# Optimization experiments

Measured on AMD Instinct MI355X. Metric: run time of the kernel, lower is better.

## Reference

```python
import jax, jax.numpy as jnp
import numpy as np

B, S, E = 8, 1024, 512
H = 8            # num_heads
D = E // H       # head_dim
FFN = 2048
WINDOW = 5       # local_window_size
EPS = 1e-5


def _mha(x, in_w, in_b, out_w, out_b, mask=None):
    """PyTorch nn.MultiheadAttention (batch_first) forward. mask: True = blocked."""
    b, s, e = x.shape
    qkv = x @ in_w.T + in_b                      # [B,S,3E]
    q, k, v = jnp.split(qkv, 3, axis=-1)
    def heads(t):
        return t.reshape(b, s, H, D).transpose(0, 2, 1, 3)  # [B,H,S,D]
    q, k, v = heads(q), heads(k), heads(v)
    scores = jnp.einsum('bhsd,bhtd->bhst', q, k) / np.sqrt(D).astype(x.dtype)
    if mask is not None:
        scores = jnp.where(mask[None, None], -jnp.inf, scores)
    attn = jax.nn.softmax(scores, axis=-1)
    out = jnp.einsum('bhst,bhtd->bhsd', attn, v)  # [B,H,S,D]
    out = out.transpose(0, 2, 1, 3).reshape(b, s, e)
    return out @ out_w.T + out_b


def _layernorm(x, g, b):
    mu = jnp.mean(x, axis=-1, keepdims=True)
    var = jnp.mean(jnp.square(x - mu), axis=-1, keepdims=True)
    return (x - mu) * jax.lax.rsqrt(var + EPS) * g + b


def setup_inputs() -> dict:
    key = jax.random.key(0)
    ks = jax.random.split(key, 8)
    w = 0.02  # weight scale for numerical sanity
    return {
        'x': jax.random.normal(ks[0], (B, S, E), jnp.float32),
        'l_in_w': jax.random.normal(ks[1], (3 * E, E), jnp.float32) * w,
        'l_in_b': jnp.zeros((3 * E,), jnp.float32),
        'l_out_w': jax.random.normal(ks[2], (E, E), jnp.float32) * w,
        'l_out_b': jnp.zeros((E,), jnp.float32),
        'g_in_w': jax.random.normal(ks[3], (3 * E, E), jnp.float32) * w,
        'g_in_b': jnp.zeros((3 * E,), jnp.float32),
        'g_out_w': jax.random.normal(ks[4], (E, E), jnp.float32) * w,
        'g_out_b': jnp.zeros((E,), jnp.float32),
        'ffn_w1': jax.random.normal(ks[5], (FFN, E), jnp.float32) * w,
        'ffn_b1': jnp.zeros((FFN,), jnp.float32),
        'ffn_w2': jax.random.normal(ks[6], (E, FFN), jnp.float32) * w,
        'ffn_b2': jnp.zeros((E,), jnp.float32),
        'ln1_g': jnp.ones((E,), jnp.float32),
        'ln1_b': jnp.zeros((E,), jnp.float32),
        'ln2_g': jnp.ones((E,), jnp.float32),
        'ln2_b': jnp.zeros((E,), jnp.float32),
    }


def reference(x, l_in_w, l_in_b, l_out_w, l_out_b,
              g_in_w, g_in_b, g_out_w, g_out_b,
              ffn_w1, ffn_b1, ffn_w2, ffn_b2,
              ln1_g, ln1_b, ln2_g, ln2_b):
    s = x.shape[1]
    idx = jnp.arange(s)
    local_mask = jnp.abs(idx[:, None] - idx[None, :]) > WINDOW  # True = blocked
    local_out = _mha(x, l_in_w, l_in_b, l_out_w, l_out_b, mask=local_mask)
    global_out = _mha(x, g_in_w, g_in_b, g_out_w, g_out_b)
    x = x + local_out + global_out
    x = _layernorm(x, ln1_g, ln1_b)
    ffn = jax.nn.relu(x @ ffn_w1.T + ffn_b1) @ ffn_w2.T + ffn_b2
    x = _layernorm(x + ffn, ln2_g, ln2_b)
    return x
```

## Files before the change

### kernel.cpp

```cpp
#include <hip/hip_runtime.h>
#include <hip/hip_bf16.h>
#include <stdint.h>

#define Bb 8
#define Ss 1024
#define Ee 512
#define Hh 8
#define Dh 64
#define FFNd 2048
#define EPSv 1e-5f

typedef float f32x4 __attribute__((ext_vector_type(4)));
typedef int   i32x4 __attribute__((ext_vector_type(4)));

__device__ inline float bf2f(ushort u) {
    uint32_t x = ((uint32_t)u) << 16; float f; __builtin_memcpy(&f, &x, 4); return f;
}
__device__ inline ushort f2bf(float f) {
    uint32_t x; __builtin_memcpy(&x, &f, 4);
    uint32_t r = (x + 0x7FFFu + ((x >> 16) & 1u)) >> 16; return (ushort)r;
}

__device__ inline void gload16(const ushort* g, ushort* l) {
    __builtin_amdgcn_global_load_lds((const __attribute__((address_space(1))) void*)g,
                                     (__attribute__((address_space(3))) void*)l,
                                     16, 0, 0);
}

__global__ void cvt_f32_bf16(const float* __restrict__ in, ushort* __restrict__ out, int n4) {
    int i = blockIdx.x * blockDim.x + threadIdx.x;
    if (i < n4) {
        float4 v = ((const float4*)in)[i];
        ushort4 o;
        o.x = f2bf(v.x); o.y = f2bf(v.y); o.z = f2bf(v.z); o.w = f2bf(v.w);
        ((ushort4*)out)[i] = o;
    }
}

template<bool OUT_BF16, bool RELU>
__global__ __launch_bounds__(256) void gemm_bt(const ushort* __restrict__ A,
                                               const ushort* __restrict__ Bm,
                                               const float* __restrict__ bias,
                                               void* __restrict__ C,
                                               int M, int N, int K) {
    __shared__ ushort Alds[128 * 32];
    __shared__ ushort Blds[128 * 32];
    int tid  = threadIdx.x;
    int lane = tid & 63, w = tid >> 6;
    int wr = w >> 1, wc = w & 1;
    int g  = lane >> 4, fr = lane & 15;
    int m0 = blockIdx.y * 128, n0 = blockIdx.x * 128;

    int lr4 = lane >> 2;
    int lc8 = (lane & 3) * 8;
    const ushort* gA0 = A  + (size_t)(m0 + (w * 2) * 16 + lr4) * K + lc8;
    const ushort* gA1 = gA0 + (size_t)16 * K;
    const ushort* gB0 = Bm + (size_t)(n0 + (w * 2) * 16 + lr4) * K + lc8;
    const ushort* gB1 = gB0 + (size_t)16 * K;
    ushort* lA0 = Alds + (w * 2) * 16 * 32;
    ushort* lA1 = lA0 + 16 * 32;
    ushort* lB0 = Blds + (w * 2) * 16 * 32;
    ushort* lB1 = lB0 + 16 * 32;

    f32x4 acc[4][4] = {};

    for (int kb = 0; kb < K; kb += 32) {
        __syncthreads();
        gload16(gA0 + kb, lA0);
        gload16(gA1 + kb, lA1);
        gload16(gB0 + kb, lB0);
        gload16(gB1 + kb, lB1);
        __syncthreads();
        i32x4 af[4], bfr[4];
        #pragma unroll
        for (int mt = 0; mt < 4; ++mt)
            af[mt] = *(const i32x4*)(Alds + (wr * 64 + mt * 16 + fr) * 32 + g * 8);
        #pragma unroll
        for (int nt = 0; nt < 4; ++nt)
            bfr[nt] = *(const i32x4*)(Blds + (wc * 64 + nt * 16 + fr) * 32 + g * 8);
        #pragma unroll
        for (int mt = 0; mt < 4; ++mt)
            #pragma unroll
            for (int nt = 0; nt < 4; ++nt)
                asm("v_mfma_f32_16x16x32_bf16 %0, %1, %2, %0"
                    : "+v"(acc[mt][nt]) : "v"(af[mt]), "v"(bfr[nt]));
    }

    #pragma unroll
    for (int mt = 0; mt < 4; ++mt) {
        int r0 = m0 + wr * 64 + mt * 16 + g * 4;
        #pragma unroll
        for (int nt = 0; nt < 4; ++nt) {
            int c = n0 + wc * 64 + nt * 16 + fr;
            float bv = bias[c];
            #pragma unroll
            for (int r = 0; r < 4; ++r) {
                float v = acc[mt][nt][r] + bv;
                if (RELU) v = v > 0.f ? v : 0.f;
                if (OUT_BF16) ((ushort*)C)[(size_t)(r0 + r) * N + c] = f2bf(v);
                else          ((float*)C)[(size_t)(r0 + r) * N + c] = v;
            }
        }
    }
}

__global__ __launch_bounds__(256) void attn_local_mfma(const ushort* __restrict__ qkv,
                                                       ushort* __restrict__ out) {
    __shared__ ushort Klds[64 * 64];
    __shared__ ushort Vtlds[64 * 64];
    __shared__ ushort Plds[4][32 * 64];
    int tid  = threadIdx.x;
    int lane = tid & 63, w = tid >> 6;
    int fr = lane & 15, g = lane >> 4;
    int qtile = blockIdx.x & 7;
    int bh = blockIdx.x >> 3;
    int h = bh & 7, b = bh >> 3;
    const size_t bbase = (size_t)b * Ss * (3 * Ee);
    const ushort* qp = qkv + bbase + h * Dh;
    const ushort* kbase = qkv + bbase + Ee + h * Dh;
    const ushort* vbase = qkv + bbase + 2 * Ee + h * Dh;

    i32x4 qf[2][2];
    int q0 = qtile * 128 + w * 32;
    #pragma unroll
    for (int mt = 0; mt < 2; ++mt)
        #pragma unroll
        for (int kb = 0; kb < 2; ++kb)
            qf[mt][kb] = *(const i32x4*)(qp + (size_t)(q0 + mt * 16 + fr) * (3 * Ee) + kb * 32 + g * 8);

    f32x4 oacc[2][4] = {};
    f32x4 lsum[2] = {};
    ushort* Pw = Plds[w];

    int tq2 = qtile * 2;
    int kt0 = tq2 > 0 ? tq2 - 1 : 0;
    int kt1 = tq2 + 2 < 16 ? tq2 + 2 : 15;
    for (int kt = kt0; kt <= kt1; ++kt) {
        int kv0 = kt * 64;
        i32x4 kr[2], vr[2];
        #pragma unroll
        for (int u = 0; u < 2; ++u) {
            int c = tid + u * 256;
            int row = c >> 3, col8 = c & 7;
            kr[u] = *(const i32x4*)(kbase + (size_t)(kv0 + row) * (3 * Ee) + col8 * 8);
            vr[u] = *(const i32x4*)(vbase + (size_t)(kv0 + row) * (3 * Ee) + col8 * 8);
        }
        __syncthreads();
        #pragma unroll
        for (int u = 0; u < 2; ++u) {
            int c = tid + u * 256;
            int row = c >> 3, col8 = c & 7;
            int kidx = (row * 64 + col8 * 8) ^ ((row & 7) << 3);
            *(i32x4*)(Klds + kidx) = kr[u];
            ushort tmp[8];
            *(i32x4*)tmp = vr[u];
            #pragma unroll
            for (int j = 0; j < 8; ++j) {
                int d = col8 * 8 + j;
                Vtlds[(d * 64 + row) ^ ((d & 7) << 3)] = tmp[j];
            }
        }
        __syncthreads();

        bool active = (kv0 <= q0 + 36) && (kv0 + 63 >= q0 - 5);
        if (active) {
            f32x4 sacc[2][4] = {};
            i32x4 kf[4][2];
            #pragma unroll
            for (int nt = 0; nt < 4; ++nt) {
                int kvl = nt * 16 + fr;
                #pragma unroll
                for (int kb = 0; kb < 2; ++kb)
                    kf[nt][kb] = *(const i32x4*)(Klds + ((kvl * 64 + kb * 32 + g * 8) ^ ((kvl & 7) << 3)));
            }
            #pragma unroll
            for (int mt = 0; mt < 2; ++mt)
                #pragma unroll
                for (int nt = 0; nt < 4; ++nt)
                    #pragma unroll
                    for (int kb = 0; kb < 2; ++kb)
                        asm("v_mfma_f32_16x16x32_bf16 %0, %1, %2, %0"
                            : "+v"(sacc[mt][nt]) : "v"(qf[mt][kb]), "v"(kf[nt][kb]));

            #pragma unroll
            for (int mt = 0; mt < 2; ++mt) {
                #pragma unroll
                for (int r = 0; r < 4; ++r) {
                    int ql = mt * 16 + g * 4 + r;
                    int sw = (ql & 7) << 3;
                    int d0 = (q0 + ql) - (kv0 + fr);
                    int d1 = d0 - 16, d2 = d0 - 32, d3 = d0 - 48;
                    float e0 = (d0 >= -5 && d0 <= 5) ? __expf(sacc[mt][0][r] * 0.125f) : 0.f;
                    float e1 = (d1 >= -5 && d1 <= 5) ? __expf(sacc[mt][1][r] * 0.125f) : 0.f;
                    float e2 = (d2 >= -5 && d2 <= 5) ? __expf(sacc[mt][2][r] * 0.125f) : 0.f;
                    float e3 = (d3 >= -5 && d3 <= 5) ? __expf(sacc[mt][3][r] * 0.125f) : 0.f;
                    Pw[(ql * 64 +  0 + fr) ^ sw] = f2bf(e0);
                    Pw[(ql * 64 + 16 + fr) ^ sw] = f2bf(e1);
                    Pw[(ql * 64 + 32 + fr) ^ sw] = f2bf(e2);
                    Pw[(ql * 64 + 48 + fr) ^ sw] = f2bf(e3);
                    lsum[mt][r] += (e0 + e1) + (e2 + e3);
                }
            }

            i32x4 pa[2][2], vf[4][2];
            #pragma unroll
            for (int mt = 0; mt < 2; ++mt) {
                int ql = mt * 16 + fr;
                #pragma unroll
                for (int kb = 0; kb < 2; ++kb)
                    pa[mt][kb] = *(const i32x4*)(Pw + ((ql * 64 + kb * 32 + g * 8) ^ ((ql & 7) << 3)));
            }
            #pragma unroll
            for (int dn = 0; dn < 4; ++dn) {
                int d = dn * 16 + fr;
                #pragma unroll
                for (int kb = 0; kb < 2; ++kb)
                    vf[dn][kb] = *(const i32x4*)(Vtlds + ((d * 64 + kb * 32 + g * 8) ^ ((d & 7) << 3)));
            }
            #pragma unroll
            for (int mt = 0; mt < 2; ++mt)
                #pragma unroll
                for (int dn = 0; dn < 4; ++dn)
                    #pragma unroll
                    for (int kb = 0; kb < 2; ++kb)
                        asm("v_mfma_f32_16x16x32_bf16 %0, %1, %2, %0"
                            : "+v"(oacc[mt][dn]) : "v"(pa[mt][kb]), "v"(vf[dn][kb]));
        }
    }

    #pragma unroll
    for (int mt = 0; mt < 2; ++mt)
        #pragma unroll
        for (int r = 0; r < 4; ++r) {
            float s = lsum[mt][r];
            s += __shfl_xor(s, 1); s += __shfl_xor(s, 2);
            s += __shfl_xor(s, 4); s += __shfl_xor(s, 8);
            lsum[mt][r] = 1.f / s;
        }

    #pragma unroll
    for (int mt = 0; mt < 2; ++mt)
        #pragma unroll
        for (int r = 0; r < 4; ++r) {
            int qg = q0 + mt * 16 + g * 4 + r;
            size_t ob = (size_t)(b * Ss + qg) * Ee + h * Dh;
            #pragma unroll
            for (int dn = 0; dn < 4; ++dn)
                out[ob + dn * 16 + fr] = f2bf(oacc[mt][dn][r] * lsum[mt][r]);
        }
}

__global__ __launch_bounds__(256) void attn_global_mfma(const ushort* __restrict__ qkv,
                                                        ushort* __restrict__ out) {
    __shared__ ushort Klds[64 * 64];
    __shared__ ushort Vtlds[64 * 64];
    __shared__ ushort Plds[4][32 * 64];
    int tid  = threadIdx.x;
    int lane = tid & 63, w = tid >> 6;
    int fr = lane & 15, g = lane >> 4;
    int qtile = blockIdx.x & 7;
    int bh = blockIdx.x >> 3;
    int h = bh & 7, b = bh >> 3;
    const size_t bbase = (size_t)b * Ss * (3 * Ee);
    const ushort* qp = qkv + bbase + h * Dh;
    const ushort* kbase = qkv + bbase + Ee + h * Dh;
    const ushort* vbase = qkv + bbase + 2 * Ee + h * Dh;

    i32x4 qf[2][2];
    int q0 = qtile * 128 + w * 32;
    #pragma unroll
    for (int mt = 0; mt < 2; ++mt)
        #pragma unroll
        for (int kb = 0; kb < 2; ++kb)
            qf[mt][kb] = *(const i32x4*)(qp + (size_t)(q0 + mt * 16 + fr) * (3 * Ee) + kb * 32 + g * 8);

    f32x4 oacc[2][4] = {};
    f32x4 lsum[2] = {};
    ushort* Pw = Plds[w];

    for (int kt = 0; kt < 16; ++kt) {
        int kv0 = kt * 64;
        i32x4 kr[2], vr[2];
        #pragma unroll
        for (int u = 0; u < 2; ++u) {
            int c = tid + u * 256;
            int row = c >> 3, col8 = c & 7;
            kr[u] = *(const i32x4*)(kbase + (size_t)(kv0 + row) * (3 * Ee) + col8 * 8);
            vr[u] = *(const i32x4*)(vbase + (size_t)(kv0 + row) * (3 * Ee) + col8 * 8);
        }
        __syncthreads();
        #pragma unroll
        for (int u = 0; u < 2; ++u) {
            int c = tid + u * 256;
            int row = c >> 3, col8 = c & 7;
            int kidx = (row * 64 + col8 * 8) ^ ((row & 7) << 3);
            *(i32x4*)(Klds + kidx) = kr[u];
            ushort tmp[8];
            *(i32x4*)tmp = vr[u];
            #pragma unroll
            for (int j = 0; j < 8; ++j) {
                int d = col8 * 8 + j;
                Vtlds[(d * 64 + row) ^ ((d & 7) << 3)] = tmp[j];
            }
        }
        __syncthreads();

        f32x4 sacc[2][4] = {};
        i32x4 kf[4][2];
        #pragma unroll
        for (int nt = 0; nt < 4; ++nt) {
            int kvl = nt * 16 + fr;
            #pragma unroll
            for (int kb = 0; kb < 2; ++kb)
                kf[nt][kb] = *(const i32x4*)(Klds + ((kvl * 64 + kb * 32 + g * 8) ^ ((kvl & 7) << 3)));
        }
        #pragma unroll
        for (int mt = 0; mt < 2; ++mt)
            #pragma unroll
            for (int nt = 0; nt < 4; ++nt)
                #pragma unroll
                for (int kb = 0; kb < 2; ++kb)
                    asm("v_mfma_f32_16x16x32_bf16 %0, %1, %2, %0"
                        : "+v"(sacc[mt][nt]) : "v"(qf[mt][kb]), "v"(kf[nt][kb]));

        #pragma unroll
        for (int mt = 0; mt < 2; ++mt) {
            #pragma unroll
            for (int r = 0; r < 4; ++r) {
                int ql = mt * 16 + g * 4 + r;
                int sw = (ql & 7) << 3;
                float e0 = __expf(sacc[mt][0][r] * 0.125f);
                float e1 = __expf(sacc[mt][1][r] * 0.125f);
                float e2 = __expf(sacc[mt][2][r] * 0.125f);
                float e3 = __expf(sacc[mt][3][r] * 0.125f);
                Pw[(ql * 64 +  0 + fr) ^ sw] = f2bf(e0);
                Pw[(ql * 64 + 16 + fr) ^ sw] = f2bf(e1);
                Pw[(ql * 64 + 32 + fr) ^ sw] = f2bf(e2);
                Pw[(ql * 64 + 48 + fr) ^ sw] = f2bf(e3);
                lsum[mt][r] += (e0 + e1) + (e2 + e3);
            }
        }

        i32x4 pa[2][2], vf[4][2];
        #pragma unroll
        for (int mt = 0; mt < 2; ++mt) {
            int ql = mt * 16 + fr;
            #pragma unroll
            for (int kb = 0; kb < 2; ++kb)
                pa[mt][kb] = *(const i32x4*)(Pw + ((ql * 64 + kb * 32 + g * 8) ^ ((ql & 7) << 3)));
        }
        #pragma unroll
        for (int dn = 0; dn < 4; ++dn) {
            int d = dn * 16 + fr;
            #pragma unroll
            for (int kb = 0; kb < 2; ++kb)
                vf[dn][kb] = *(const i32x4*)(Vtlds + ((d * 64 + kb * 32 + g * 8) ^ ((d & 7) << 3)));
        }
        #pragma unroll
        for (int mt = 0; mt < 2; ++mt)
            #pragma unroll
            for (int dn = 0; dn < 4; ++dn)
                #pragma unroll
                for (int kb = 0; kb < 2; ++kb)
                    asm("v_mfma_f32_16x16x32_bf16 %0, %1, %2, %0"
                        : "+v"(oacc[mt][dn]) : "v"(pa[mt][kb]), "v"(vf[dn][kb]));
    }

    #pragma unroll
    for (int mt = 0; mt < 2; ++mt)
        #pragma unroll
        for (int r = 0; r < 4; ++r) {
            float s = lsum[mt][r];
            s += __shfl_xor(s, 1); s += __shfl_xor(s, 2);
            s += __shfl_xor(s, 4); s += __shfl_xor(s, 8);
            lsum[mt][r] = 1.f / s;
        }

    #pragma unroll
    for (int mt = 0; mt < 2; ++mt)
        #pragma unroll
        for (int r = 0; r < 4; ++r) {
            int qg = q0 + mt * 16 + g * 4 + r;
            size_t ob = (size_t)(b * Ss + qg) * Ee + h * Dh;
            #pragma unroll
            for (int dn = 0; dn < 4; ++dn)
                out[ob + dn * 16 + fr] = f2bf(oacc[mt][dn][r] * lsum[mt][r]);
        }
}

__global__ __launch_bounds__(256) void ln_add3(const float* __restrict__ x,
                                               const float* __restrict__ p1,
                                               const float* __restrict__ p2,
                                               const float* __restrict__ gam,
                                               const float* __restrict__ bet,
                                               ushort* __restrict__ yb,
                                               float* __restrict__ yf) {
    int row  = blockIdx.x * 4 + (threadIdx.x >> 6);
    int lane = threadIdx.x & 63;
    size_t off = (size_t)row * Ee + lane * 8;
    float hv[8];
    float4 a0 = *(const float4*)(x + off),  a1 = *(const float4*)(x + off + 4);
    float4 b0 = *(const float4*)(p1 + off), b1 = *(const float4*)(p1 + off + 4);
    float4 c0 = *(const float4*)(p2 + off), c1 = *(const float4*)(p2 + off + 4);
    hv[0] = a0.x + b0.x + c0.x; hv[1] = a0.y + b0.y + c0.y;
    hv[2] = a0.z + b0.z + c0.z; hv[3] = a0.w + b0.w + c0.w;
    hv[4] = a1.x + b1.x + c1.x; hv[5] = a1.y + b1.y + c1.y;
    hv[6] = a1.z + b1.z + c1.z; hv[7] = a1.w + b1.w + c1.w;
    float s = 0.f;
    #pragma unroll
    for (int i = 0; i < 8; ++i) s += hv[i];
    #pragma unroll
    for (int o = 32; o; o >>= 1) s += __shfl_xor(s, o);
    float mu = s * (1.f / Ee);
    float vs = 0.f;
    #pragma unroll
    for (int i = 0; i < 8; ++i) { float d = hv[i] - mu; vs += d * d; }
    #pragma unroll
    for (int o = 32; o; o >>= 1) vs += __shfl_xor(vs, o);
    float rs = rsqrtf(vs * (1.f / Ee) + EPSv);
    #pragma unroll
    for (int i = 0; i < 8; ++i) {
        float yv = (hv[i] - mu) * rs * gam[lane * 8 + i] + bet[lane * 8 + i];
        yf[off + i] = yv;
        yb[off + i] = f2bf(yv);
    }
}

__global__ __launch_bounds__(256) void ln_add2(const float* __restrict__ a,
                                               const float* __restrict__ bsrc,
                                               const float* __restrict__ gam,
                                               const float* __restrict__ bet,
                                               float* __restrict__ outp) {
    int row  = blockIdx.x * 4 + (threadIdx.x >> 6);
    int lane = threadIdx.x & 63;
    size_t off = (size_t)row * Ee + lane * 8;
    float hv[8];
    float4 a0 = *(const float4*)(a + off),    a1 = *(const float4*)(a + off + 4);
    float4 b0 = *(const float4*)(bsrc + off), b1 = *(const float4*)(bsrc + off + 4);
    hv[0] = a0.x + b0.x; hv[1] = a0.y + b0.y; hv[2] = a0.z + b0.z; hv[3] = a0.w + b0.w;
    hv[4] = a1.x + b1.x; hv[5] = a1.y + b1.y; hv[6] = a1.z + b1.z; hv[7] = a1.w + b1.w;
    float s = 0.f;
    #pragma unroll
    for (int i = 0; i < 8; ++i) s += hv[i];
    #pragma unroll
    for (int o = 32; o; o >>= 1) s += __shfl_xor(s, o);
    float mu = s * (1.f / Ee);
    float vs = 0.f;
    #pragma unroll
    for (int i = 0; i < 8; ++i) { float d = hv[i] - mu; vs += d * d; }
    #pragma unroll
    for (int o = 32; o; o >>= 1) vs += __shfl_xor(vs, o);
    float rs = rsqrtf(vs * (1.f / Ee) + EPSv);
    #pragma unroll
    for (int i = 0; i < 8; ++i)
        outp[off + i] = (hv[i] - mu) * rs * gam[lane * 8 + i] + bet[lane * 8 + i];
}

extern "C" void kernel_launch(void* const* d_in, const int* in_sizes, int n_in,
                              void* d_out, int out_size, void* d_ws, size_t ws_size,
                              hipStream_t stream) {
    const float* x      = (const float*)d_in[0];
    const float* l_in_w = (const float*)d_in[1];
    const float* l_in_b = (const float*)d_in[2];
    const float* l_out_w= (const float*)d_in[3];
    const float* l_out_b= (const float*)d_in[4];
    const float* g_in_w = (const float*)d_in[5];
    const float* g_in_b = (const float*)d_in[6];
    const float* g_out_w= (const float*)d_in[7];
    const float* g_out_b= (const float*)d_in[8];
    const float* ffn_w1 = (const float*)d_in[9];
    const float* ffn_b1 = (const float*)d_in[10];
    const float* ffn_w2 = (const float*)d_in[11];
    const float* ffn_b2 = (const float*)d_in[12];
    const float* ln1_g  = (const float*)d_in[13];
    const float* ln1_b  = (const float*)d_in[14];
    const float* ln2_g  = (const float*)d_in[15];
    const float* ln2_b  = (const float*)d_in[16];

    char* ws = (char*)d_ws;
    ushort* xb       = (ushort*)(ws + 0);
    ushort* wb       = (ushort*)(ws + 8388608);
    ushort* l_in_wb  = wb;
    ushort* g_in_wb  = wb + 786432;
    ushort* l_out_wb = wb + 1572864;
    ushort* g_out_wb = wb + 1835008;
    ushort* w1b      = wb + 2097152;
    ushort* w2b      = wb + 3145728;
    ushort* qkvLb    = (ushort*)(ws + 16777216);
    ushort* qkvGb    = (ushort*)(ws + 41943040);
    ushort* attnLb   = (ushort*)(ws + 67108864);
    ushort* attnGb   = (ushort*)(ws + 75497472);
    float*  projL    = (float*)(ws + 16777216);
    float*  projG    = (float*)(ws + 33554432);
    ushort* y1b      = (ushort*)(ws + 50331648);
    float*  y1f      = (float*)(ws + 58720256);
    ushort* ffn1b    = (ushort*)(ws + 16777216);
    float*  ffn2f    = (float*)(ws + 75497472);

    const int M = Bb * Ss;

    auto cvt = [&](const float* in, ushort* out, int n) {
        int n4 = n / 4;
        cvt_f32_bf16<<<dim3((n4 + 255) / 256), dim3(256), 0, stream>>>(in, out, n4);
    };
    cvt(x,       xb,       Bb * Ss * Ee);
    cvt(l_in_w,  l_in_wb,  3 * Ee * Ee);
    cvt(g_in_w,  g_in_wb,  3 * Ee * Ee);
    cvt(l_out_w, l_out_wb, Ee * Ee);
    cvt(g_out_w, g_out_wb, Ee * Ee);
    cvt(ffn_w1,  w1b,      FFNd * Ee);
    cvt(ffn_w2,  w2b,      Ee * FFNd);

    gemm_bt<true, false><<<dim3((3 * Ee) / 128, M / 128), 256, 0, stream>>>(
        xb, l_in_wb, l_in_b, qkvLb, M, 3 * Ee, Ee);
    gemm_bt<true, false><<<dim3((3 * Ee) / 128, M / 128), 256, 0, stream>>>(
        xb, g_in_wb, g_in_b, qkvGb, M, 3 * Ee, Ee);

    attn_local_mfma<<<dim3(Bb * Hh * (Ss / 128)), 256, 0, stream>>>(qkvLb, attnLb);
    attn_global_mfma<<<dim3(Bb * Hh * (Ss / 128)), 256, 0, stream>>>(qkvGb, attnGb);

    gemm_bt<false, false><<<dim3(Ee / 128, M / 128), 256, 0, stream>>>(
        attnLb, l_out_wb, l_out_b, projL, M, Ee, Ee);
    gemm_bt<false, false><<<dim3(Ee / 128, M / 128), 256, 0, stream>>>(
        attnGb, g_out_wb, g_out_b, projG, M, Ee, Ee);

    ln_add3<<<dim3(M / 4), 256, 0, stream>>>(x, projL, projG, ln1_g, ln1_b, y1b, y1f);

    gemm_bt<true, true><<<dim3(FFNd / 128, M / 128), 256, 0, stream>>>(
        y1b, w1b, ffn_b1, ffn1b, M, FFNd, Ee);
    gemm_bt<false, false><<<dim3(Ee / 128, M / 128), 256, 0, stream>>>(
        ffn1b, w2b, ffn_b2, ffn2f, M, Ee, FFNd);

    ln_add2<<<dim3(M / 4), 256, 0, stream>>>(y1f, ffn2f, ln2_g, ln2_b, (float*)d_out);
}
```

Baseline: 339.4 us.

## Fuse QKV projections and conversions, prefetch K/V tiles, improve V swizzle

Merges the seven f32-to-bf16 conversion launches into one kernel, and merges the local and global QKV projections into a single N=3072 GEMM. The GEMM takes a second bias pointer selected by column, and both attention kernels read from the shared QKV buffer with a 3072 stride. Both attention kernels now prefetch the next K/V tile into registers while computing on the current one. The transposed-V LDS layout uses a two-level XOR swizzle to cut bank conflicts. This removes launch overhead and improves overlap, at the cost of more register pressure in the attention kernels.

Result: faster. 319.0 us (-6.0%).

```diff
diff --git a/kernel.cpp b/kernel.cpp
--- a/kernel.cpp
+++ b/kernel.cpp
@@ -9,6 +9,7 @@
 #define Dh 64
 #define FFNd 2048
 #define EPSv 1e-5f
+#define QS 3072
 
 typedef float f32x4 __attribute__((ext_vector_type(4)));
 typedef int   i32x4 __attribute__((ext_vector_type(4)));
@@ -27,20 +28,36 @@
                                      16, 0, 0);
 }
 
-__global__ void cvt_f32_bf16(const float* __restrict__ in, ushort* __restrict__ out, int n4) {
-    int i = blockIdx.x * blockDim.x + threadIdx.x;
-    if (i < n4) {
-        float4 v = ((const float4*)in)[i];
-        ushort4 o;
-        o.x = f2bf(v.x); o.y = f2bf(v.y); o.z = f2bf(v.z); o.w = f2bf(v.w);
-        ((ushort4*)out)[i] = o;
-    }
+__device__ inline int vswz(int d, int kv) {
+    return (d * 64 + kv) ^ ((((d & 7) ^ ((d >> 3) & 7)) & 7) << 3);
+}
+
+__global__ __launch_bounds__(256) void cvt_all(const float* __restrict__ s0, const float* __restrict__ s1,
+                                               const float* __restrict__ s2, const float* __restrict__ s3,
+                                               const float* __restrict__ s4, const float* __restrict__ s5,
+                                               const float* __restrict__ s6,
+                                               ushort* __restrict__ dx, ushort* __restrict__ dw) {
+    int bid = blockIdx.x;
+    const float* src; ushort* dst; int boff;
+    if (bid < 4096)      { src = s0; dst = dx;            boff = bid; }
+    else if (bid < 4864) { src = s1; dst = dw;            boff = bid - 4096; }
+    else if (bid < 5632) { src = s2; dst = dw + 786432;   boff = bid - 4864; }
+    else if (bid < 5888) { src = s3; dst = dw + 1572864;  boff = bid - 5632; }
+    else if (bid < 6144) { src = s4; dst = dw + 1835008;  boff = bid - 5888; }
+    else if (bid < 7168) { src = s5; dst = dw + 2097152;  boff = bid - 6144; }
+    else                 { src = s6; dst = dw + 3145728;  boff = bid - 7168; }
+    int i = boff * 256 + threadIdx.x;
+    float4 v = ((const float4*)src)[i];
+    ushort4 o;
+    o.x = f2bf(v.x); o.y = f2bf(v.y); o.z = f2bf(v.z); o.w = f2bf(v.w);
+    ((ushort4*)dst)[i] = o;
 }
 
 template<bool OUT_BF16, bool RELU>
 __global__ __launch_bounds__(256) void gemm_bt(const ushort* __restrict__ A,
                                                const ushort* __restrict__ Bm,
                                                const float* __restrict__ bias,
+                                               const float* __restrict__ bias2, int nb1,
                                                void* __restrict__ C,
                                                int M, int N, int K) {
     __shared__ ushort Alds[128 * 32];
@@ -92,7 +109,7 @@
         #pragma unroll
         for (int nt = 0; nt < 4; ++nt) {
             int c = n0 + wc * 64 + nt * 16 + fr;
-            float bv = bias[c];
+            float bv = c < nb1 ? bias[c] : bias2[c - nb1];
             #pragma unroll
             for (int r = 0; r < 4; ++r) {
                 float v = acc[mt][nt][r] + bv;
@@ -102,6 +119,145 @@
             }
         }
     }
+}
+
+__global__ __launch_bounds__(256) void attn_global_mfma(const ushort* __restrict__ qkv,
+                                                        ushort* __restrict__ out) {
+    __shared__ ushort Klds[64 * 64];
+    __shared__ ushort Vtlds[64 * 64];
+    __shared__ ushort Plds[4][32 * 64];
+    int tid  = threadIdx.x;
+    int lane = tid & 63, w = tid >> 6;
+    int fr = lane & 15, g = lane >> 4;
+    int qtile = blockIdx.x & 7;
+    int bh = blockIdx.x >> 3;
+    int h = bh & 7, b = bh >> 3;
+    const ushort* qp    = qkv + (size_t)b * Ss * QS + h * Dh;
+    const ushort* kbase = qp + Ee;
+    const ushort* vbase = qp + 2 * Ee;
+
+    i32x4 qf[2][2];
+    int q0 = qtile * 128 + w * 32;
+    #pragma unroll
+    for (int mt = 0; mt < 2; ++mt)
+        #pragma unroll
+        for (int kb = 0; kb < 2; ++kb)
+            qf[mt][kb] = *(const i32x4*)(qp + (size_t)(q0 + mt * 16 + fr) * QS + kb * 32 + g * 8);
+
+    f32x4 oacc[2][4] = {};
+    f32x4 lsum[2] = {};
+    ushort* Pw = Plds[w];
+
+    i32x4 kr[2], vr[2];
+    auto load_tile = [&](int kv0) {
+        #pragma unroll
+        for (int u = 0; u < 2; ++u) {
+            int c = tid + u * 256;
+            int row = c >> 3, col8 = c & 7;
+            kr[u] = *(const i32x4*)(kbase + (size_t)(kv0 + row) * QS + col8 * 8);
+            vr[u] = *(const i32x4*)(vbase + (size_t)(kv0 + row) * QS + col8 * 8);
+        }
+    };
+    load_tile(0);
+
+    for (int kt = 0; kt < 16; ++kt) {
+        __syncthreads();
+        #pragma unroll
+        for (int u = 0; u < 2; ++u) {
+            int c = tid + u * 256;
+            int row = c >> 3, col8 = c & 7;
+            int kidx = (row * 64 + col8 * 8) ^ ((row & 7) << 3);
+            *(i32x4*)(Klds + kidx) = kr[u];
+            ushort tmp[8];
+            *(i32x4*)tmp = vr[u];
+            #pragma unroll
+            for (int j = 0; j < 8; ++j)
+                Vtlds[vswz(col8 * 8 + j, row)] = tmp[j];
+        }
+        __syncthreads();
+        if (kt < 15) load_tile((kt + 1) * 64);
+
+        f32x4 sacc[2][4] = {};
+        i32x4 kf[4][2];
+        #pragma unroll
+        for (int nt = 0; nt < 4; ++nt) {
+            int kvl = nt * 16 + fr;
+            #pragma unroll
+            for (int kb = 0; kb < 2; ++kb)
+                kf[nt][kb] = *(const i32x4*)(Klds + ((kvl * 64 + kb * 32 + g * 8) ^ ((kvl & 7) << 3)));
+        }
+        #pragma unroll
+        for (int mt = 0; mt < 2; ++mt)
+            #pragma unroll
+            for (int nt = 0; nt < 4; ++nt)
+                #pragma unroll
+                for (int kb = 0; kb < 2; ++kb)
+                    asm("v_mfma_f32_16x16x32_bf16 %0, %1, %2, %0"
+                        : "+v"(sacc[mt][nt]) : "v"(qf[mt][kb]), "v"(kf[nt][kb]));
+
+        #pragma unroll
+        for (int mt = 0; mt < 2; ++mt) {
+            #pragma unroll
+            for (int r = 0; r < 4; ++r) {
+                int ql = mt * 16 + g * 4 + r;
+                int sw = (ql & 7) << 3;
+                float e0 = __expf(sacc[mt][0][r] * 0.125f);
+                float e1 = __expf(sacc[mt][1][r] * 0.125f);
+                float e2 = __expf(sacc[mt][2][r] * 0.125f);
+                float e3 = __expf(sacc[mt][3][r] * 0.125f);
+                Pw[(ql * 64 +  0 + fr) ^ sw] = f2bf(e0);
+                Pw[(ql * 64 + 16 + fr) ^ sw] = f2bf(e1);
+                Pw[(ql * 64 + 32 + fr) ^ sw] = f2bf(e2);
+                Pw[(ql * 64 + 48 + fr) ^ sw] = f2bf(e3);
+                lsum[mt][r] += (e0 + e1) + (e2 + e3);
+            }
+        }
+
+        i32x4 pa[2][2], vf[4][2];
+        #pragma unroll
+        for (int mt = 0; mt < 2; ++mt) {
+            int ql = mt * 16 + fr;
+            #pragma unroll
+            for (int kb = 0; kb < 2; ++kb)
+                pa[mt][kb] = *(const i32x4*)(Pw + ((ql * 64 + kb * 32 + g * 8) ^ ((ql & 7) << 3)));
+        }
+        #pragma unroll
+        for (int dn = 0; dn < 4; ++dn) {
+            int d = dn * 16 + fr;
+            #pragma unroll
+            for (int kb = 0; kb < 2; ++kb)
+                vf[dn][kb] = *(const i32x4*)(Vtlds + vswz(d, kb * 32 + g * 8));
+        }
+        #pragma unroll
+        for (int mt = 0; mt < 2; ++mt)
+            #pragma unroll
+            for (int dn = 0; dn < 4; ++dn)
+                #pragma unroll
+                for (int kb = 0; kb < 2; ++kb)
+                    asm("v_mfma_f32_16x16x32_bf16 %0, %1, %2, %0"
+                        : "+v"(oacc[mt][dn]) : "v"(pa[mt][kb]), "v"(vf[dn][kb]));
+    }
+
+    #pragma unroll
+    for (int mt = 0; mt < 2; ++mt)
+        #pragma unroll
+        for (int r = 0; r < 4; ++r) {
+            float s = lsum[mt][r];
+            s += __shfl_xor(s, 1); s += __shfl_xor(s, 2);
+            s += __shfl_xor(s, 4); s += __shfl_xor(s, 8);
+            lsum[mt][r] = 1.f / s;
+        }
+
+    #pragma unroll
+    for (int mt = 0; mt < 2; ++mt)
+        #pragma unroll
+        for (int r = 0; r < 4; ++r) {
+            int qg = q0 + mt * 16 + g * 4 + r;
+            size_t ob = (size_t)(b * Ss + qg) * Ee + h * Dh;
+            #pragma unroll
+            for (int dn = 0; dn < 4; ++dn)
+                out[ob + dn * 16 + fr] = f2bf(oacc[mt][dn][r] * lsum[mt][r]);
+        }
 }
 
 __global__ __launch_bounds__(256) void attn_local_mfma(const ushort* __restrict__ qkv,
@@ -115,10 +271,9 @@
     int qtile = blockIdx.x & 7;
     int bh = blockIdx.x >> 3;
     int h = bh & 7, b = bh >> 3;
-    const size_t bbase = (size_t)b * Ss * (3 * Ee);
-    const ushort* qp = qkv + bbase + h * Dh;
-    const ushort* kbase = qkv + bbase + Ee + h * Dh;
-    const ushort* vbase = qkv + bbase + 2 * Ee + h * Dh;
+    const ushort* qp    = qkv + (size_t)b * Ss * QS + h * Dh;
+    const ushort* kbase = qp + Ee;
+    const ushort* vbase = qp + 2 * Ee;
 
     i32x4 qf[2][2];
     int q0 = qtile * 128 + w * 32;
@@ -126,25 +281,30 @@
     for (int mt = 0; mt < 2; ++mt)
         #pragma unroll
         for (int kb = 0; kb < 2; ++kb)
-            qf[mt][kb] = *(const i32x4*)(qp + (size_t)(q0 + mt * 16 + fr) * (3 * Ee) + kb * 32 + g * 8);
+            qf[mt][kb] = *(const i32x4*)(qp + (size_t)(q0 + mt * 16 + fr) * QS + kb * 32 + g * 8);
 
     f32x4 oacc[2][4] = {};
     f32x4 lsum[2] = {};
     ushort* Pw = Plds[w];
 
+    i32x4 kr[2], vr[2];
+    auto load_tile = [&](int kv0) {
+        #pragma unroll
+        for (int u = 0; u < 2; ++u) {
+            int c = tid + u * 256;
+            int row = c >> 3, col8 = c & 7;
+            kr[u] = *(const i32x4*)(kbase + (size_t)(kv0 + row) * QS + col8 * 8);
+            vr[u] = *(const i32x4*)(vbase + (size_t)(kv0 + row) * QS + col8 * 8);
+        }
+    };
+
     int tq2 = qtile * 2;
     int kt0 = tq2 > 0 ? tq2 - 1 : 0;
     int kt1 = tq2 + 2 < 16 ? tq2 + 2 : 15;
+    load_tile(kt0 * 64);
+
     for (int kt = kt0; kt <= kt1; ++kt) {
         int kv0 = kt * 64;
-        i32x4 kr[2], vr[2];
-        #pragma unroll
-        for (int u = 0; u < 2; ++u) {
-            int c = tid + u * 256;
-            int row = c >> 3, col8 = c & 7;
-            kr[u] = *(const i32x4*)(kbase + (size_t)(kv0 + row) * (3 * Ee) + col8 * 8);
-            vr[u] = *(const i32x4*)(vbase + (size_t)(kv0 + row) * (3 * Ee) + col8 * 8);
-        }
         __syncthreads();
         #pragma unroll
         for (int u = 0; u < 2; ++u) {
@@ -155,12 +315,11 @@
             ushort tmp[8];
             *(i32x4*)tmp = vr[u];
             #pragma unroll
-            for (int j = 0; j < 8; ++j) {
-                int d = col8 * 8 + j;
-                Vtlds[(d * 64 + row) ^ ((d & 7) << 3)] = tmp[j];
-            }
+            for (int j = 0; j < 8; ++j)
+                Vtlds[vswz(col8 * 8 + j, row)] = tmp[j];
         }
         __syncthreads();
+        if (kt < kt1) load_tile((kt + 1) * 64);
 
         bool active = (kv0 <= q0 + 36) && (kv0 + 63 >= q0 - 5);
         if (active) {
@@ -215,7 +374,7 @@
                 int d = dn * 16 + fr;
                 #pragma unroll
                 for (int kb = 0; kb < 2; ++kb)
-                    vf[dn][kb] = *(const i32x4*)(Vtlds + ((d * 64 + kb * 32 + g * 8) ^ ((d & 7) << 3)));
+                    vf[dn][kb] = *(const i32x4*)(Vtlds + vswz(d, kb * 32 + g * 8));
             }
             #pragma unroll
             for (int mt = 0; mt < 2; ++mt)
@@ -226,144 +385,6 @@
                         asm("v_mfma_f32_16x16x32_bf16 %0, %1, %2, %0"
                             : "+v"(oacc[mt][dn]) : "v"(pa[mt][kb]), "v"(vf[dn][kb]));
         }
-    }
-
-    #pragma unroll
-    for (int mt = 0; mt < 2; ++mt)
-        #pragma unroll
-        for (int r = 0; r < 4; ++r) {
-            float s = lsum[mt][r];
-            s += __shfl_xor(s, 1); s += __shfl_xor(s, 2);
-            s += __shfl_xor(s, 4); s += __shfl_xor(s, 8);
-            lsum[mt][r] = 1.f / s;
-        }
-
-    #pragma unroll
-    for (int mt = 0; mt < 2; ++mt)
-        #pragma unroll
-        for (int r = 0; r < 4; ++r) {
-            int qg = q0 + mt * 16 + g * 4 + r;
-            size_t ob = (size_t)(b * Ss + qg) * Ee + h * Dh;
-            #pragma unroll
-            for (int dn = 0; dn < 4; ++dn)
-                out[ob + dn * 16 + fr] = f2bf(oacc[mt][dn][r] * lsum[mt][r]);
-        }
-}
-
-__global__ __launch_bounds__(256) void attn_global_mfma(const ushort* __restrict__ qkv,
-                                                        ushort* __restrict__ out) {
-    __shared__ ushort Klds[64 * 64];
-    __shared__ ushort Vtlds[64 * 64];
-    __shared__ ushort Plds[4][32 * 64];
-    int tid  = threadIdx.x;
-    int lane = tid & 63, w = tid >> 6;
-    int fr = lane & 15, g = lane >> 4;
-    int qtile = blockIdx.x & 7;
-    int bh = blockIdx.x >> 3;
-    int h = bh & 7, b = bh >> 3;
-    const size_t bbase = (size_t)b * Ss * (3 * Ee);
-    const ushort* qp = qkv + bbase + h * Dh;
-    const ushort* kbase = qkv + bbase + Ee + h * Dh;
-    const ushort* vbase = qkv + bbase + 2 * Ee + h * Dh;
-
-    i32x4 qf[2][2];
-    int q0 = qtile * 128 + w * 32;
-    #pragma unroll
-    for (int mt = 0; mt < 2; ++mt)
-        #pragma unroll
-        for (int kb = 0; kb < 2; ++kb)
-            qf[mt][kb] = *(const i32x4*)(qp + (size_t)(q0 + mt * 16 + fr) * (3 * Ee) + kb * 32 + g * 8);
-
-    f32x4 oacc[2][4] = {};
-    f32x4 lsum[2] = {};
-    ushort* Pw = Plds[w];
-
-    for (int kt = 0; kt < 16; ++kt) {
-        int kv0 = kt * 64;
-        i32x4 kr[2], vr[2];
-        #pragma unroll
-        for (int u = 0; u < 2; ++u) {
-            int c = tid + u * 256;
-            int row = c >> 3, col8 = c & 7;
-            kr[u] = *(const i32x4*)(kbase + (size_t)(kv0 + row) * (3 * Ee) + col8 * 8);
-            vr[u] = *(const i32x4*)(vbase + (size_t)(kv0 + row) * (3 * Ee) + col8 * 8);
-        }
-        __syncthreads();
-        #pragma unroll
-        for (int u = 0; u < 2; ++u) {
-            int c = tid + u * 256;
-            int row = c >> 3, col8 = c & 7;
-            int kidx = (row * 64 + col8 * 8) ^ ((row & 7) << 3);
-            *(i32x4*)(Klds + kidx) = kr[u];
-            ushort tmp[8];
-            *(i32x4*)tmp = vr[u];
-            #pragma unroll
-            for (int j = 0; j < 8; ++j) {
-                int d = col8 * 8 + j;
-                Vtlds[(d * 64 + row) ^ ((d & 7) << 3)] = tmp[j];
-            }
-        }
-        __syncthreads();
-
-        f32x4 sacc[2][4] = {};
-        i32x4 kf[4][2];
-        #pragma unroll
-        for (int nt = 0; nt < 4; ++nt) {
-            int kvl = nt * 16 + fr;
-            #pragma unroll
-            for (int kb = 0; kb < 2; ++kb)
-                kf[nt][kb] = *(const i32x4*)(Klds + ((kvl * 64 + kb * 32 + g * 8) ^ ((kvl & 7) << 3)));
-        }
-        #pragma unroll
-        for (int mt = 0; mt < 2; ++mt)
-            #pragma unroll
-            for (int nt = 0; nt < 4; ++nt)
-                #pragma unroll
-                for (int kb = 0; kb < 2; ++kb)
-                    asm("v_mfma_f32_16x16x32_bf16 %0, %1, %2, %0"
-                        : "+v"(sacc[mt][nt]) : "v"(qf[mt][kb]), "v"(kf[nt][kb]));
-
-        #pragma unroll
-        for (int mt = 0; mt < 2; ++mt) {
-            #pragma unroll
-            for (int r = 0; r < 4; ++r) {
-                int ql = mt * 16 + g * 4 + r;
-                int sw = (ql & 7) << 3;
-                float e0 = __expf(sacc[mt][0][r] * 0.125f);
-                float e1 = __expf(sacc[mt][1][r] * 0.125f);
-                float e2 = __expf(sacc[mt][2][r] * 0.125f);
-                float e3 = __expf(sacc[mt][3][r] * 0.125f);
-                Pw[(ql * 64 +  0 + fr) ^ sw] = f2bf(e0);
-                Pw[(ql * 64 + 16 + fr) ^ sw] = f2bf(e1);
-                Pw[(ql * 64 + 32 + fr) ^ sw] = f2bf(e2);
-                Pw[(ql * 64 + 48 + fr) ^ sw] = f2bf(e3);
-                lsum[mt][r] += (e0 + e1) + (e2 + e3);
-            }
-        }
-
-        i32x4 pa[2][2], vf[4][2];
-        #pragma unroll
-        for (int mt = 0; mt < 2; ++mt) {
-            int ql = mt * 16 + fr;
-            #pragma unroll
-            for (int kb = 0; kb < 2; ++kb)
-                pa[mt][kb] = *(const i32x4*)(Pw + ((ql * 64 + kb * 32 + g * 8) ^ ((ql & 7) << 3)));
-        }
-        #pragma unroll
-        for (int dn = 0; dn < 4; ++dn) {
-            int d = dn * 16 + fr;
-            #pragma unroll
-            for (int kb = 0; kb < 2; ++kb)
-                vf[dn][kb] = *(const i32x4*)(Vtlds + ((d * 64 + kb * 32 + g * 8) ^ ((d & 7) << 3)));
-        }
-        #pragma unroll
-        for (int mt = 0; mt < 2; ++mt)
-            #pragma unroll
-            for (int dn = 0; dn < 4; ++dn)
-                #pragma unroll
-                for (int kb = 0; kb < 2; ++kb)
-                    asm("v_mfma_f32_16x16x32_bf16 %0, %1, %2, %0"
-                        : "+v"(oacc[mt][dn]) : "v"(pa[mt][kb]), "v"(vf[dn][kb]));
     }
 
     #pragma unroll
@@ -480,14 +501,11 @@
     char* ws = (char*)d_ws;
     ushort* xb       = (ushort*)(ws + 0);
     ushort* wb       = (ushort*)(ws + 8388608);
-    ushort* l_in_wb  = wb;
-    ushort* g_in_wb  = wb + 786432;
     ushort* l_out_wb = wb + 1572864;
-    ushort* g_out_wb = wb + 1835008;
     ushort* w1b      = wb + 2097152;
     ushort* w2b      = wb + 3145728;
-    ushort* qkvLb    = (ushort*)(ws + 16777216);
-    ushort* qkvGb    = (ushort*)(ws + 41943040);
+    ushort* g_out_wb = wb + 1835008;
+    ushort* qkvb     = (ushort*)(ws + 16777216);
     ushort* attnLb   = (ushort*)(ws + 67108864);
     ushort* attnGb   = (ushort*)(ws + 75497472);
     float*  projL    = (float*)(ws + 16777216);
@@ -499,37 +517,26 @@
 
     const int M = Bb * Ss;
 
-    auto cvt = [&](const float* in, ushort* out, int n) {
-        int n4 = n / 4;
-        cvt_f32_bf16<<<dim3((n4 + 255) / 256), dim3(256), 0, stream>>>(in, out, n4);
-    };
-    cvt(x,       xb,       Bb * Ss * Ee);
-    cvt(l_in_w,  l_in_wb,  3 * Ee * Ee);
-    cvt(g_in_w,  g_in_wb,  3 * Ee * Ee);
-    cvt(l_out_w, l_out_wb, Ee * Ee);
-    cvt(g_out_w, g_out_wb, Ee * Ee);
-    cvt(ffn_w1,  w1b,      FFNd * Ee);
-    cvt(ffn_w2,  w2b,      Ee * FFNd);
-
-    gemm_bt<true, false><<<dim3((3 * Ee) / 128, M / 128), 256, 0, stream>>>(
-        xb, l_in_wb, l_in_b, qkvLb, M, 3 * Ee, Ee);
-    gemm_bt<true, false><<<dim3((3 * Ee) / 128, M / 128), 256, 0, stream>>>(
-        xb, g_in_wb, g_in_b, qkvGb, M, 3 * Ee, Ee);
-
-    attn_local_mfma<<<dim3(Bb * Hh * (Ss / 128)), 256, 0, stream>>>(qkvLb, attnLb);
-    attn_global_mfma<<<dim3(Bb * Hh * (Ss / 128)), 256, 0, stream>>>(qkvGb, attnGb);
-
-    gemm_bt<false, false><<<dim3(Ee / 128, M / 128), 256, 0, stream>>>(
-        attnLb, l_out_wb, l_out_b, projL, M, Ee, Ee);
-    gemm_bt<false, false><<<dim3(Ee / 128, M / 128), 256, 0, stream>>>(
-        attnGb, g_out_wb, g_out_b, projG, M, Ee, Ee);
+    cvt_all<<<dim3(8192), dim3(256), 0, stream>>>(x, l_in_w, g_in_w, l_out_w, g_out_w,
+                                                  ffn_w1, ffn_w2, xb, wb);
+
+    gemm_bt<true, false><<<dim3(24, 64), 256, 0, stream>>>(
+        xb, wb, l_in_b, g_in_b, 1536, qkvb, M, QS, Ee);
+
+    attn_local_mfma<<<dim3(Bb * Hh * (Ss / 128)), 256, 0, stream>>>(qkvb, attnLb);
+    attn_global_mfma<<<dim3(Bb * Hh * (Ss / 128)), 256, 0, stream>>>(qkvb + 1536, attnGb);
+
+    gemm_bt<false, false><<<dim3(4, 64), 256, 0, stream>>>(
+        attnLb, l_out_wb, l_out_b, l_out_b, Ee, projL, M, Ee, Ee);
+    gemm_bt<false, false><<<dim3(4, 64), 256, 0, stream>>>(
+        attnGb, g_out_wb, g_out_b, g_out_b, Ee, projG, M, Ee, Ee);
 
     ln_add3<<<dim3(M / 4), 256, 0, stream>>>(x, projL, projG, ln1_g, ln1_b, y1b, y1f);
 
-    gemm_bt<true, true><<<dim3(FFNd / 128, M / 128), 256, 0, stream>>>(
-        y1b, w1b, ffn_b1, ffn1b, M, FFNd, Ee);
-    gemm_bt<false, false><<<dim3(Ee / 128, M / 128), 256, 0, stream>>>(
-        ffn1b, w2b, ffn_b2, ffn2f, M, Ee, FFNd);
+    gemm_bt<true, true><<<dim3(16, 64), 256, 0, stream>>>(
+        y1b, w1b, ffn_b1, ffn_b1, FFNd, ffn1b, M, FFNd, Ee);
+    gemm_bt<false, false><<<dim3(4, 64), 256, 0, stream>>>(
+        ffn1b, w2b, ffn_b2, ffn_b2, Ee, ffn2f, M, Ee, FFNd);
 
     ln_add2<<<dim3(M / 4), 256, 0, stream>>>(y1f, ffn2f, ln2_g, ln2_b, (float*)d_out);
 }
```
